# Performance work log

Measured on AMD Instinct MI355X. Metric: run time of the kernel, lower is better.

## Reference

```python
import jax, jax.numpy as jnp
import numpy as np
import math

D_MODEL = 512
N_HEADS = 8
FACTOR = 5
B, L_Q, L_K = 8, 4096, 4096


def setup_inputs() -> dict:
    key = jax.random.key(0)
    ks = jax.random.split(key, 9)
    s = 0.02
    sample_k = max(1, int(FACTOR * math.log(L_K + 1)))  # 41
    return {
        "query": jax.random.normal(ks[0], (B, L_Q, D_MODEL), jnp.float32),
        "key_in": jax.random.normal(ks[1], (B, L_K, D_MODEL), jnp.float32),
        "value": jax.random.normal(ks[2], (B, L_K, D_MODEL), jnp.float32),
        "W_Q": jax.random.normal(ks[3], (D_MODEL, D_MODEL), jnp.float32) * s,
        "W_K": jax.random.normal(ks[4], (D_MODEL, D_MODEL), jnp.float32) * s,
        "W_V": jax.random.normal(ks[5], (D_MODEL, D_MODEL), jnp.float32) * s,
        "W_out": jax.random.normal(ks[6], (D_MODEL, D_MODEL), jnp.float32) * s,
        "b_out": jnp.zeros((D_MODEL,), jnp.float32),
        "sample_idx": jax.random.randint(ks[8], (L_Q, sample_k), 0, L_K),
    }


def reference(query, key_in, value, W_Q, W_K, W_V, W_out, b_out, sample_idx):
    b, lq, _ = query.shape
    lk = key_in.shape[1]
    H = N_HEADS
    E = D_MODEL // H
    # projections -> [B, H, L, E]
    Q = (query @ W_Q).reshape(b, lq, H, E).transpose(0, 2, 1, 3)
    K = (key_in @ W_K).reshape(b, lk, H, E).transpose(0, 2, 1, 3)
    V = (value @ W_V).reshape(b, lk, H, E).transpose(0, 2, 1, 3)

    u = max(1, int(FACTOR * math.log(lq + 1)))  # top-u queries (41)

    # sparsity proxy M(q_i, K) on randomly sampled keys
    K_sample = K[:, :, sample_idx, :]                      # [B,H,L_Q,S,E]
    QK_sample = jnp.einsum('bhqe,bhqse->bhqs', Q, K_sample)
    M = QK_sample.max(axis=-1) - QK_sample.mean(axis=-1)   # [B,H,L_Q]
    _, M_top = jax.lax.top_k(M, u)                         # [B,H,u]

    # attention for the top-u queries only
    Q_reduce = jnp.take_along_axis(Q, M_top[..., None], axis=2)  # [B,H,u,E]
    scale = 1.0 / math.sqrt(E)
    scores = jnp.einsum('bhue,bhke->bhuk', Q_reduce, K) * scale
    attn = jax.nn.softmax(scores, axis=-1)  # dropout is identity (eval)
    ctx_top = jnp.einsum('bhuk,bhke->bhue', attn, V)       # [B,H,u,E]

    # mean-value context for the lazy queries, scatter-update the active ones
    ctx = jnp.broadcast_to(V.mean(axis=2, keepdims=True), (b, H, lq, E))
    bi = jnp.arange(b)[:, None, None]
    hi = jnp.arange(H)[None, :, None]
    ctx = ctx.at[bi, hi, M_top].set(ctx_top)

    ctx = ctx.transpose(0, 2, 1, 3).reshape(b, lq, H * E)
    return ctx @ W_out + b_out
```

## Files before the change

### kernel.cpp

```cpp
#include <hip/hip_runtime.h>
#include <cstdint>
#include <cstddef>

#define D_MODEL 512
#define NHEADS  8
#define EDIM    64
#define BATCH   8
#define LSEQ    4096

typedef unsigned short u16;
typedef __attribute__((ext_vector_type(8))) short short8;
typedef __attribute__((ext_vector_type(4))) float f32x4;

__device__ __forceinline__ u16 bf16_rne(float x) {
  unsigned int u = __float_as_uint(x);
  u += 0x7FFFu + ((u >> 16) & 1u);
  return (u16)(u >> 16);
}
__device__ __forceinline__ void split2(float x, u16& h, u16& l) {
  h = bf16_rne(x);
  float hf = __uint_as_float((unsigned int)h << 16);
  l = bf16_rne(x - hf);
}

__global__ __launch_bounds__(256) void cvt_w(
    const float* __restrict__ W0, const float* __restrict__ W1,
    const float* __restrict__ W2, const float* __restrict__ W3,
    u16* __restrict__ out) {
  const float* W = (blockIdx.z == 0) ? W0 : ((blockIdx.z == 1) ? W1 :
                   ((blockIdx.z == 2) ? W2 : W3));
  u16* P = out + (size_t)blockIdx.z * 524288;
  __shared__ float tile[64][65];
  const int k0 = blockIdx.x * 64, n0 = blockIdx.y * 64;
  const int t = threadIdx.x;
  const int tr = t >> 4, tc = (t & 15) * 4;
#pragma unroll
  for (int j = 0; j < 4; ++j) {
    int kr = tr + j * 16;
    float4 v = *(const float4*)(W + (size_t)(k0 + kr) * 512 + n0 + tc);
    tile[kr][tc + 0] = v.x; tile[kr][tc + 1] = v.y;
    tile[kr][tc + 2] = v.z; tile[kr][tc + 3] = v.w;
  }
  __syncthreads();
#pragma unroll
  for (int j = 0; j < 4; ++j) {
    int nr = tr + j * 16;
    ushort4 h, l;
    split2(tile[tc + 0][nr], h.x, l.x);
    split2(tile[tc + 1][nr], h.y, l.y);
    split2(tile[tc + 2][nr], h.z, l.z);
    split2(tile[tc + 3][nr], h.w, l.w);
    size_t off = (size_t)(n0 + nr) * 512 + k0 + tc;
    *(ushort4*)(P + off) = h;
    *(ushort4*)(P + 262144 + off) = l;
  }
}

__device__ __forceinline__ void gld_lds16(const char* g, char* l) {
  __builtin_amdgcn_global_load_lds((const __attribute__((address_space(1))) void*)g,
                                   (__attribute__((address_space(3))) void*)l, 16, 0, 0);
}

__global__ __launch_bounds__(256, 2) void gemm_fused(
    const float* __restrict__ X, const u16* __restrict__ WP,
    float* __restrict__ Y) {
  __shared__ u16 Ah[128 * 40];
  __shared__ u16 Al[128 * 40];
  __shared__ u16 Bh[128 * 32];
  __shared__ u16 Bl[128 * 32];
  const int tid = threadIdx.x;
  const int lane = tid & 63, wv = tid >> 6;
  const int wm = (wv & 1) * 64, wn = (wv >> 1) * 64;
  const int bn = blockIdx.x * 128, bm = blockIdx.y * 128;
  const int fr = lane & 15, quad = lane >> 4;
  const int sRow = tid >> 2, sColB = (tid & 3) * 16;
  const int ar = tid >> 1, ac = (tid & 1) * 16;

  f32x4 acc[16];
#pragma unroll
  for (int i = 0; i < 16; ++i) acc[i] = (f32x4){0.f, 0.f, 0.f, 0.f};

  const u16* Wh = WP;
  const u16* Wl = WP + 262144;
  const float* Arow = X + (size_t)(bm + ar) * 512 + ac;

  union V8 { ushort4 v4[2]; short8 v8; };

  for (int kk = 0; kk < 16; ++kk) {
    float4 x0 = *(const float4*)(Arow + kk * 32);
    float4 x1 = *(const float4*)(Arow + kk * 32 + 4);
    float4 x2 = *(const float4*)(Arow + kk * 32 + 8);
    float4 x3 = *(const float4*)(Arow + kk * 32 + 12);
#pragma unroll
    for (int j = 0; j < 2; ++j) {
      const size_t rB = (size_t)(bn + j * 64 + sRow) * 512 + kk * 32;
      const int lo = (j * 256 + wv * 64) * 16;
      gld_lds16((const char*)(Wh + rB) + sColB, (char*)Bh + lo);
      gld_lds16((const char*)(Wl + rB) + sColB, (char*)Bl + lo);
    }
    V8 h0, l0, h1, l1;
    split2(x0.x, h0.v4[0].x, l0.v4[0].x);
    split2(x0.y, h0.v4[0].y, l0.v4[0].y);
    split2(x0.z, h0.v4[0].z, l0.v4[0].z);
    split2(x0.w, h0.v4[0].w, l0.v4[0].w);
    split2(x1.x, h0.v4[1].x, l0.v4[1].x);
    split2(x1.y, h0.v4[1].y, l0.v4[1].y);
    split2(x1.z, h0.v4[1].z, l0.v4[1].z);
    split2(x1.w, h0.v4[1].w, l0.v4[1].w);
    split2(x2.x, h1.v4[0].x, l1.v4[0].x);
    split2(x2.y, h1.v4[0].y, l1.v4[0].y);
    split2(x2.z, h1.v4[0].z, l1.v4[0].z);
    split2(x2.w, h1.v4[0].w, l1.v4[0].w);
    split2(x3.x, h1.v4[1].x, l1.v4[1].x);
    split2(x3.y, h1.v4[1].y, l1.v4[1].y);
    split2(x3.z, h1.v4[1].z, l1.v4[1].z);
    split2(x3.w, h1.v4[1].w, l1.v4[1].w);
    *(short8*)&Ah[ar * 40 + ac]     = h0.v8;
    *(short8*)&Ah[ar * 40 + ac + 8] = h1.v8;
    *(short8*)&Al[ar * 40 + ac]     = l0.v8;
    *(short8*)&Al[ar * 40 + ac + 8] = l1.v8;
    __syncthreads();
    short8 ah[4], al[4], bh[4], bl[4];
#pragma unroll
    for (int mi = 0; mi < 4; ++mi) {
      ah[mi] = *(const short8*)&Ah[(wm + mi * 16 + fr) * 40 + quad * 8];
      al[mi] = *(const short8*)&Al[(wm + mi * 16 + fr) * 40 + quad * 8];
    }
#pragma unroll
    for (int ni = 0; ni < 4; ++ni) {
      bh[ni] = *(const short8*)&Bh[(wn + ni * 16 + fr) * 32 + quad * 8];
      bl[ni] = *(const short8*)&Bl[(wn + ni * 16 + fr) * 32 + quad * 8];
    }
#pragma unroll
    for (int mi = 0; mi < 4; ++mi)
#pragma unroll
      for (int ni = 0; ni < 4; ++ni)
        acc[mi * 4 + ni] = __builtin_amdgcn_mfma_f32_16x16x32_bf16(
            ah[mi], bh[ni], acc[mi * 4 + ni], 0, 0, 0);
#pragma unroll
    for (int mi = 0; mi < 4; ++mi)
#pragma unroll
      for (int ni = 0; ni < 4; ++ni)
        acc[mi * 4 + ni] = __builtin_amdgcn_mfma_f32_16x16x32_bf16(
            ah[mi], bl[ni], acc[mi * 4 + ni], 0, 0, 0);
#pragma unroll
    for (int mi = 0; mi < 4; ++mi)
#pragma unroll
      for (int ni = 0; ni < 4; ++ni)
        acc[mi * 4 + ni] = __builtin_amdgcn_mfma_f32_16x16x32_bf16(
            al[mi], bh[ni], acc[mi * 4 + ni], 0, 0, 0);
    __syncthreads();
  }
#pragma unroll
  for (int mi = 0; mi < 4; ++mi)
#pragma unroll
    for (int ni = 0; ni < 4; ++ni) {
      const f32x4 a = acc[mi * 4 + ni];
      float* yp = Y + (size_t)(bm + wm + mi * 16 + quad * 4) * 512 + (bn + wn + ni * 16 + fr);
#pragma unroll
      for (int r = 0; r < 4; ++r) yp[(size_t)r * 512] = a[r];
    }
}

__global__ __launch_bounds__(256) void qk_sample_half(
    const float* __restrict__ Q, const float* __restrict__ K,
    const int* __restrict__ sidx, float* __restrict__ M, int S, int hg) {
  const int blk = blockIdx.x;
  const int lane = threadIdx.x & 63;
  const int b = blk & 7;
  const int q = ((blk >> 3) << 2) + (threadIdx.x >> 6);
  const int s = lane >> 5;
  const int hl = (lane >> 3) & 3;
  const int d = lane & 7;
  const int h = hg * 4 + hl;
  const int col = hg * 256 + hl * 64 + d * 8;

  const float* Qp = Q + ((size_t)b * LSEQ + q) * D_MODEL + col;
  const float4 q0 = *(const float4*)Qp;
  const float4 q1 = *(const float4*)(Qp + 4);
  const float* Kb = K + (size_t)b * LSEQ * D_MODEL + col;
  const int* sp = sidx + (size_t)q * S;

  auto spclamp = [&](int j) -> int {
    int jj = j + s;
    return sp[(jj < S) ? jj : (S - 1)];
  };

  int i0 = spclamp(0), i1 = spclamp(2), i2 = spclamp(4), i3 = spclamp(6);
  const float* p0 = Kb + (size_t)i0 * D_MODEL;
  float4 a0 = *(const float4*)p0, b0 = *(const float4*)(p0 + 4);
  const float* p1 = Kb + (size_t)i1 * D_MODEL;
  float4 a1 = *(const float4*)p1, b1 = *(const float4*)(p1 + 4);
  const float* p2 = Kb + (size_t)i2 * D_MODEL;
  float4 a2 = *(const float4*)p2, b2 = *(const float4*)(p2 + 4);

  float mx = -3.4e38f, sum = 0.0f;
  for (int j = 0; j < S; j += 2) {
    const float4 ca = a0, cb = b0;
    a0 = a1; b0 = b1; a1 = a2; b1 = b2;
    const float* pn = Kb + (size_t)i3 * D_MODEL;
    a2 = *(const float4*)pn;
    b2 = *(const float4*)(pn + 4);
    i3 = spclamp(j + 8);
    float p = ca.x * q0.x + ca.y * q0.y + ca.z * q0.z + ca.w * q0.w +
              cb.x * q1.x + cb.y * q1.y + cb.z * q1.z + cb.w * q1.w;
    p += __shfl_xor(p, 1, 64);
    p += __shfl_xor(p, 2, 64);
    p += __shfl_xor(p, 4, 64);
    if (j + s < S) {
      mx = fmaxf(mx, p);
      sum += p;
    }
  }
  mx = fmaxf(mx, __shfl_xor(mx, 32, 64));
  sum += __shfl_xor(sum, 32, 64);
  if (s == 0 && d == 0)
    M[((size_t)(b * NHEADS + h)) * LSEQ + q] = mx - sum / (float)S;
}

__global__ __launch_bounds__(256) void topk_kernel(
    const float* __restrict__ M, int* __restrict__ Mtop, int U) {
  __shared__ float vals[LSEQ];
  __shared__ float rmax[256];
  __shared__ int ridx[256];
  int bh = blockIdx.x;
  int t = threadIdx.x;
  for (int i = t; i < LSEQ; i += 256) vals[i] = M[(size_t)bh * LSEQ + i];
  __syncthreads();
  for (int it = 0; it < U; ++it) {
    float best = -3.4e38f; int bi = -1;
    for (int i = t; i < LSEQ; i += 256) {
      float v = vals[i];
      if (v > best) { best = v; bi = i; }
    }
    rmax[t] = best; ridx[t] = bi;
    __syncthreads();
    for (int s = 128; s > 0; s >>= 1) {
      if (t < s) {
        if (rmax[t + s] > rmax[t]) { rmax[t] = rmax[t + s]; ridx[t] = ridx[t + s]; }
      }
      __syncthreads();
    }
    if (t == 0) {
      Mtop[(size_t)bh * U + it] = ridx[0];
      vals[ridx[0]] = -3.4e38f;
    }
    __syncthreads();
  }
}

__global__ __launch_bounds__(256, 2) void attn_flash(
    const float* __restrict__ Q, const float* __restrict__ K,
    const float* __restrict__ V, const int* __restrict__ Mtop,
    float* __restrict__ part_ctx, float* __restrict__ part_m,
    float* __restrict__ part_l, int U, int nsplit, int chunks_per_block) {
  __shared__ u16 KhS[64 * 72];
  __shared__ u16 KlS[64 * 72];
  __shared__ float VsS[64 * 68];
  const int bh = blockIdx.y, split = blockIdx.x;
  const int h = bh & (NHEADS - 1), b = bh >> 3;
  const int t = threadIdx.x, w = t >> 6, lane = t & 63;
  const int fr = lane & 15, quad = lane >> 4;

  const int qi = w * 16 + fr;
  const int qrow = (qi < U) ? Mtop[(size_t)bh * U + qi] : Mtop[(size_t)bh * U];
  const float4* Qr = (const float4*)(Q + ((size_t)(b * LSEQ) + qrow) * D_MODEL + h * EDIM);
  float4 qa = Qr[quad * 2], qb = Qr[quad * 2 + 1];
  float4 qc = Qr[quad * 2 + 8], qd = Qr[quad * 2 + 9];
  short8 qh0, ql0, qh1, ql1;
  {
    u16 hh, ll;
    split2(qa.x, hh, ll); qh0[0] = (short)hh; ql0[0] = (short)ll;
    split2(qa.y, hh, ll); qh0[1] = (short)hh; ql0[1] = (short)ll;
    split2(qa.z, hh, ll); qh0[2] = (short)hh; ql0[2] = (short)ll;
    split2(qa.w, hh, ll); qh0[3] = (short)hh; ql0[3] = (short)ll;
    split2(qb.x, hh, ll); qh0[4] = (short)hh; ql0[4] = (short)ll;
    split2(qb.y, hh, ll); qh0[5] = (short)hh; ql0[5] = (short)ll;
    split2(qb.z, hh, ll); qh0[6] = (short)hh; ql0[6] = (short)ll;
    split2(qb.w, hh, ll); qh0[7] = (short)hh; ql0[7] = (short)ll;
    split2(qc.x, hh, ll); qh1[0] = (short)hh; ql1[0] = (short)ll;
    split2(qc.y, hh, ll); qh1[1] = (short)hh; ql1[1] = (short)ll;
    split2(qc.z, hh, ll); qh1[2] = (short)hh; ql1[2] = (short)ll;
    split2(qc.w, hh, ll); qh1[3] = (short)hh; ql1[3] = (short)ll;
    split2(qd.x, hh, ll); qh1[4] = (short)hh; ql1[4] = (short)ll;
    split2(qd.y, hh, ll); qh1[5] = (short)hh; ql1[5] = (short)ll;
    split2(qd.z, hh, ll); qh1[6] = (short)hh; ql1[6] = (short)ll;
    split2(qd.w, hh, ll); qh1[7] = (short)hh; ql1[7] = (short)ll;
  }

  float4 c4[16];
#pragma unroll
  for (int i = 0; i < 16; ++i) c4[i] = make_float4(0.f, 0.f, 0.f, 0.f);
  float m = -1e30f, l = 0.0f;

  const int r = t >> 2, cg = t & 3;

  const int k_base = split * (chunks_per_block * 64);
  for (int c = 0; c < chunks_per_block; ++c) {
    const int k0 = k_base + c * 64;
    const float4* Kg4 = (const float4*)(K + ((size_t)(b * LSEQ) + k0 + r) * D_MODEL + h * EDIM);
    const float4* Vg4 = (const float4*)(V + ((size_t)(b * LSEQ) + k0 + r) * D_MODEL + h * EDIM);
#pragma unroll
    for (int i = 0; i < 4; ++i) {
      const int f4 = cg + 4 * i;
      float4 kv = Kg4[f4];
      float4 vv = Vg4[f4];
      ushort4 hh, ll;
      split2(kv.x, hh.x, ll.x);
      split2(kv.y, hh.y, ll.y);
      split2(kv.z, hh.z, ll.z);
      split2(kv.w, hh.w, ll.w);
      *(ushort4*)&KhS[r * 72 + f4 * 4] = hh;
      *(ushort4*)&KlS[r * 72 + f4 * 4] = ll;
      *(float4*)&VsS[r * 68 + f4 * 4] = vv;
    }
    __syncthreads();

    f32x4 acc[4];
#pragma unroll
    for (int mt = 0; mt < 4; ++mt) acc[mt] = (f32x4){0.f, 0.f, 0.f, 0.f};
#pragma unroll
    for (int mt = 0; mt < 4; ++mt) {
      short8 kh = *(const short8*)&KhS[(mt * 16 + fr) * 72 + quad * 8];
      short8 kl = *(const short8*)&KlS[(mt * 16 + fr) * 72 + quad * 8];
      acc[mt] = __builtin_amdgcn_mfma_f32_16x16x32_bf16(kh, qh0, acc[mt], 0, 0, 0);
      acc[mt] = __builtin_amdgcn_mfma_f32_16x16x32_bf16(kh, ql0, acc[mt], 0, 0, 0);
      acc[mt] = __builtin_amdgcn_mfma_f32_16x16x32_bf16(kl, qh0, acc[mt], 0, 0, 0);
    }
#pragma unroll
    for (int mt = 0; mt < 4; ++mt) {
      short8 kh = *(const short8*)&KhS[(mt * 16 + fr) * 72 + 32 + quad * 8];
      short8 kl = *(const short8*)&KlS[(mt * 16 + fr) * 72 + 32 + quad * 8];
      acc[mt] = __builtin_amdgcn_mfma_f32_16x16x32_bf16(kh, qh1, acc[mt], 0, 0, 0);
      acc[mt] = __builtin_amdgcn_mfma_f32_16x16x32_bf16(kh, ql1, acc[mt], 0, 0, 0);
      acc[mt] = __builtin_amdgcn_mfma_f32_16x16x32_bf16(kl, qh1, acc[mt], 0, 0, 0);
    }

    float cm = -3.4e38f;
#pragma unroll
    for (int mt = 0; mt < 4; ++mt) {
#pragma unroll
      for (int rr = 0; rr < 4; ++rr) {
        float s = acc[mt][rr] * 0.125f;
        acc[mt][rr] = s;
        cm = fmaxf(cm, s);
      }
    }
    cm = fmaxf(cm, __shfl_xor(cm, 16, 64));
    cm = fmaxf(cm, __shfl_xor(cm, 32, 64));
    float mn = fmaxf(m, cm);
    if (mn > m) {
      float f = __expf(m - mn);
      l *= f;
#pragma unroll
      for (int i = 0; i < 16; ++i) {
        c4[i].x *= f; c4[i].y *= f; c4[i].z *= f; c4[i].w *= f;
      }
      m = mn;
    }
    float psum = 0.0f;
#pragma unroll
    for (int mt = 0; mt < 4; ++mt) {
#pragma unroll
      for (int rr = 0; rr < 4; ++rr) {
        float p = __expf(acc[mt][rr] - m);
        acc[mt][rr] = p;
        psum += p;
      }
    }
    l += psum;

#pragma unroll
    for (int mt = 0; mt < 4; ++mt) {
#pragma unroll
      for (int rr = 0; rr < 4; ++rr) {
        const int krow = mt * 16 + quad * 4 + rr;
        const float4* vr = (const float4*)&VsS[krow * 68];
        const float p = acc[mt][rr];
#pragma unroll
        for (int i = 0; i < 16; ++i) {
          float4 vv = vr[i];
          c4[i].x += p * vv.x; c4[i].y += p * vv.y;
          c4[i].z += p * vv.z; c4[i].w += p * vv.w;
        }
      }
    }
    __syncthreads();
  }

#pragma unroll
  for (int i = 0; i < 16; ++i) {
    c4[i].x += __shfl_xor(c4[i].x, 16, 64);
    c4[i].y += __shfl_xor(c4[i].y, 16, 64);
    c4[i].z += __shfl_xor(c4[i].z, 16, 64);
    c4[i].w += __shfl_xor(c4[i].w, 16, 64);
    c4[i].x += __shfl_xor(c4[i].x, 32, 64);
    c4[i].y += __shfl_xor(c4[i].y, 32, 64);
    c4[i].z += __shfl_xor(c4[i].z, 32, 64);
    c4[i].w += __shfl_xor(c4[i].w, 32, 64);
  }
  l += __shfl_xor(l, 16, 64);
  l += __shfl_xor(l, 32, 64);

  if (quad == 0 && qi < U) {
    part_m[(size_t)(bh * nsplit + split) * 64 + qi] = m;
    part_l[(size_t)(bh * nsplit + split) * 64 + qi] = l;
  }
  float* pc = part_ctx + (size_t)(bh * nsplit + split) * 4096;
  if (quad == 0) {
#pragma unroll
    for (int ii = 0; ii < 16; ++ii) pc[ii * 64 + qi] = (&c4[ii >> 2].x)[ii & 3];
  } else if (quad == 1) {
#pragma unroll
    for (int ii = 0; ii < 16; ++ii) pc[(16 + ii) * 64 + qi] = (&c4[4 + (ii >> 2)].x)[ii & 3];
  } else if (quad == 2) {
#pragma unroll
    for (int ii = 0; ii < 16; ++ii) pc[(32 + ii) * 64 + qi] = (&c4[8 + (ii >> 2)].x)[ii & 3];
  } else {
#pragma unroll
    for (int ii = 0; ii < 16; ++ii) pc[(48 + ii) * 64 + qi] = (&c4[12 + (ii >> 2)].x)[ii & 3];
  }
}

__global__ __launch_bounds__(256) void attn_combine(
    const float* __restrict__ part_ctx, const float* __restrict__ part_m,
    const float* __restrict__ part_l, float* __restrict__ ctxTop,
    int U, int nsplit) {
  __shared__ float F[16][64];
  const int bh = blockIdx.x;
  const int t = threadIdx.x, lane = t & 63, grp = t >> 6;
  if (grp == 0) {
    float M = -3.4e38f;
    for (int s = 0; s < nsplit; ++s)
      M = fmaxf(M, part_m[(size_t)(bh * nsplit + s) * 64 + lane]);
    float L = 0.0f;
    for (int s = 0; s < nsplit; ++s)
      L += part_l[(size_t)(bh * nsplit + s) * 64 + lane] *
           __expf(part_m[(size_t)(bh * nsplit + s) * 64 + lane] - M);
    float invL = 1.0f / L;
    for (int s = 0; s < nsplit; ++s)
      F[s][lane] = __expf(part_m[(size_t)(bh * nsplit + s) * 64 + lane] - M) * invL;
  }
  __syncthreads();
  for (int ei = 0; ei < 16; ++ei) {
    int e = grp * 16 + ei;
    float acc = 0.0f;
    for (int s = 0; s < nsplit; ++s)
      acc += F[s][lane] * part_ctx[(size_t)(bh * nsplit + s) * 4096 + e * 64 + lane];
    if (lane < U) ctxTop[((size_t)bh * U + lane) * 64 + e] = acc;
  }
}

__global__ __launch_bounds__(256) void vmean_kernel(
    const float* __restrict__ V, float* __restrict__ Vm) {
  __shared__ float part[4][EDIM];
  int bh = blockIdx.x;
  int h = bh & (NHEADS - 1), b = bh >> 3;
  int t = threadIdx.x;
  int e = t & 63, c = t >> 6;
  float s = 0.0f;
  for (int k = c * (LSEQ / 4); k < (c + 1) * (LSEQ / 4); ++k)
    s += V[((size_t)b * LSEQ + k) * D_MODEL + h * EDIM + e];
  part[c][e] = s;
  __syncthreads();
  if (c == 0)
    Vm[(size_t)bh * EDIM + e] =
        (part[0][e] + part[1][e] + part[2][e] + part[3][e]) * (1.0f / (float)LSEQ);
}

__global__ __launch_bounds__(256) void base_out_kernel(
    const float* __restrict__ Vm, const float* __restrict__ Wout,
    const float* __restrict__ bout, float* __restrict__ base) {
  __shared__ float cb[D_MODEL];
  int b = blockIdx.x;
  int t = threadIdx.x;
  for (int d = t; d < D_MODEL; d += 256) cb[d] = Vm[(size_t)b * D_MODEL + d];
  __syncthreads();
  for (int n = t; n < D_MODEL; n += 256) {
    float s = bout[n];
    for (int d = 0; d < D_MODEL; ++d) s += cb[d] * Wout[(size_t)d * D_MODEL + n];
    base[(size_t)b * D_MODEL + n] = s;
  }
}

__global__ __launch_bounds__(256) void fill_out(
    const float* __restrict__ base, float* __restrict__ out) {
  size_t i = (size_t)blockIdx.x * 256 + threadIdx.x;
  int n4 = (int)(i & 127);
  size_t bq = i >> 7;
  int b = (int)(bq >> 12);
  float4 v = ((const float4*)base)[(size_t)b * 128 + n4];
  ((float4*)out)[i] = v;
}

__global__ __launch_bounds__(256, 1) void delta_out_mfma(
    const float* __restrict__ ctxTop, const float* __restrict__ Vm,
    const int* __restrict__ Mtop, const u16* __restrict__ WoutTP,
    float* __restrict__ out, int U) {
  __shared__ u16 Dh[64 * 72];
  __shared__ u16 Dl[64 * 72];
  __shared__ int qr[64];
  const int bh = blockIdx.x;
  const int h = bh & (NHEADS - 1), b = bh >> 3;
  const int t = threadIdx.x, lane = t & 63, wv = t >> 6;
  const int fr = lane & 15, quad = lane >> 4;

  {
    const int r = t >> 2, c0 = (t & 3) * 16;
#pragma unroll
    for (int j = 0; j < 4; ++j) {
      float4 v = make_float4(0.f, 0.f, 0.f, 0.f);
      if (r < U) {
        float4 cv = *(const float4*)(ctxTop + ((size_t)bh * U + r) * EDIM + c0 + j * 4);
        float4 mv = *(const float4*)(Vm + (size_t)bh * EDIM + c0 + j * 4);
        v = make_float4(cv.x - mv.x, cv.y - mv.y, cv.z - mv.z, cv.w - mv.w);
      }
      ushort4 hh, ll;
      split2(v.x, hh.x, ll.x);
      split2(v.y, hh.y, ll.y);
      split2(v.z, hh.z, ll.z);
      split2(v.w, hh.w, ll.w);
      *(ushort4*)&Dh[r * 72 + c0 + j * 4] = hh;
      *(ushort4*)&Dl[r * 72 + c0 + j * 4] = ll;
    }
  }
  if (t < 64) qr[t] = (t < U) ? Mtop[(size_t)bh * U + t] : -1;
  __syncthreads();

  f32x4 acc[32];
#pragma unroll
  for (int i = 0; i < 32; ++i) acc[i] = (f32x4){0.f, 0.f, 0.f, 0.f};

  const u16* Wh = WoutTP;
  const u16* Wl = WoutTP + 262144;

#pragma unroll
  for (int ks = 0; ks < 2; ++ks) {
    short8 a_h[4], a_l[4];
#pragma unroll
    for (int mt = 0; mt < 4; ++mt) {
      a_h[mt] = *(const short8*)&Dh[(mt * 16 + fr) * 72 + ks * 32 + quad * 8];
      a_l[mt] = *(const short8*)&Dl[(mt * 16 + fr) * 72 + ks * 32 + quad * 8];
    }
#pragma unroll
    for (int nt = 0; nt < 8; ++nt) {
      const int n = wv * 128 + nt * 16 + fr;
      const size_t off = (size_t)n * 512 + h * EDIM + ks * 32 + quad * 8;
      short8 b_h = *(const short8*)&Wh[off];
      short8 b_l = *(const short8*)&Wl[off];
#pragma unroll
      for (int mt = 0; mt < 4; ++mt) {
        acc[mt * 8 + nt] = __builtin_amdgcn_mfma_f32_16x16x32_bf16(
            a_h[mt], b_h, acc[mt * 8 + nt], 0, 0, 0);
        acc[mt * 8 + nt] = __builtin_amdgcn_mfma_f32_16x16x32_bf16(
            a_h[mt], b_l, acc[mt * 8 + nt], 0, 0, 0);
        acc[mt * 8 + nt] = __builtin_amdgcn_mfma_f32_16x16x32_bf16(
            a_l[mt], b_h, acc[mt * 8 + nt], 0, 0, 0);
      }
    }
  }

  int qreg[16];
#pragma unroll
  for (int mt = 0; mt < 4; ++mt)
#pragma unroll
    for (int r4 = 0; r4 < 4; ++r4) qreg[mt * 4 + r4] = qr[mt * 16 + quad * 4 + r4];
#pragma unroll
  for (int mt = 0; mt < 4; ++mt)
#pragma unroll
    for (int nt = 0; nt < 8; ++nt) {
      const f32x4 a = acc[mt * 8 + nt];
      const int n = wv * 128 + nt * 16 + fr;
#pragma unroll
      for (int r4 = 0; r4 < 4; ++r4) {
        const int q = qreg[mt * 4 + r4];
        if (q >= 0)
          atomicAdd(out + ((size_t)b * LSEQ + q) * D_MODEL + n, a[r4]);
      }
    }
}

extern "C" void kernel_launch(void* const* d_in, const int* in_sizes, int n_in,
                              void* d_out, int out_size, void* d_ws, size_t ws_size,
                              hipStream_t stream) {
  const float* query  = (const float*)d_in[0];
  const float* key_in = (const float*)d_in[1];
  const float* value  = (const float*)d_in[2];
  const float* W_Q    = (const float*)d_in[3];
  const float* W_K    = (const float*)d_in[4];
  const float* W_V    = (const float*)d_in[5];
  const float* W_out  = (const float*)d_in[6];
  const float* b_out  = (const float*)d_in[7];
  const int*   sidx   = (const int*)d_in[8];
  float* out = (float*)d_out;

  const int S = in_sizes[8] / LSEQ;
  const int U = S;

  char* ws = (char*)d_ws;
  size_t o = 0;
  float* Qf     = (float*)(ws + o); o += (size_t)BATCH * LSEQ * D_MODEL * 4;
  float* Kf     = (float*)(ws + o); o += (size_t)BATCH * LSEQ * D_MODEL * 4;
  float* Vf     = (float*)(ws + o); o += (size_t)BATCH * LSEQ * D_MODEL * 4;
  int*   Mtop   = (int*)  (ws + o); o += ((size_t)64 * U * 4 + 255) & ~255ULL;
  float* ctxTop = (float*)(ws + o); o += ((size_t)64 * U * EDIM * 4 + 255) & ~255ULL;
  float* Vm     = (float*)(ws + o); o += 16384;
  float* baseO  = (float*)(ws + o); o += 16384;
  u16*   Wpl    = (u16*)  (ws + o); o += (size_t)4 * 524288 * 2;
  size_t unionOff = o;

  float* M = (float*)(ws + unionOff);
  int nsplit = 16;
  for (;;) {
    size_t need = unionOff + 2 * ((size_t)64 * nsplit * 64 * 4)
                  + (size_t)64 * nsplit * 4096 * 4;
    if (need <= ws_size || nsplit == 1) break;
    nsplit >>= 1;
  }
  float* part_m   = (float*)(ws + unionOff);
  float* part_l   = part_m + (size_t)64 * nsplit * 64;
  float* part_ctx = part_l + (size_t)64 * nsplit * 64;
  const int chunks_per_block = 64 / nsplit;

  cvt_w<<<dim3(8, 8, 4), 256, 0, stream>>>(W_Q, W_K, W_V, W_out, Wpl);
  gemm_fused<<<dim3(4, 256), 256, 0, stream>>>(query,  Wpl,                       Qf);
  gemm_fused<<<dim3(4, 256), 256, 0, stream>>>(key_in, Wpl + (size_t)1 * 524288,  Kf);
  gemm_fused<<<dim3(4, 256), 256, 0, stream>>>(value,  Wpl + (size_t)2 * 524288,  Vf);

  qk_sample_half<<<(BATCH * LSEQ) / 4, 256, 0, stream>>>(Qf, Kf, sidx, M, S, 0);
  qk_sample_half<<<(BATCH * LSEQ) / 4, 256, 0, stream>>>(Qf, Kf, sidx, M, S, 1);
  topk_kernel<<<BATCH * NHEADS, 256, 0, stream>>>(M, Mtop, U);
  attn_flash<<<dim3(nsplit, BATCH * NHEADS), 256, 0, stream>>>(
      Qf, Kf, Vf, Mtop, part_ctx, part_m, part_l, U, nsplit, chunks_per_block);
  attn_combine<<<BATCH * NHEADS, 256, 0, stream>>>(
      part_ctx, part_m, part_l, ctxTop, U, nsplit);
  vmean_kernel<<<BATCH * NHEADS, 256, 0, stream>>>(Vf, Vm);
  base_out_kernel<<<BATCH, 256, 0, stream>>>(Vm, W_out, b_out, baseO);
  fill_out<<<(BATCH * LSEQ * (D_MODEL / 4)) / 256, 256, 0, stream>>>(baseO, out);
  delta_out_mfma<<<BATCH * NHEADS, 256, 0, stream>>>(
      ctxTop, Vm, Mtop, Wpl + (size_t)3 * 524288, out, U);
}
```

Before: 779.2 us.

## Double-buffer projection GEMM, merge QKV launches, speed up topk and vmean

The projection GEMM now double-buffers its LDS tiles so the next K-slice's global loads and bf16 split run alongside the MFMAs of the current slice. The three Q/K/V GEMMs are merged into one launch through blockIdx.z. The top-k selection replaces its shared-memory tree reduction with wave shuffles and explicit tie-breaking. The V-mean kernel is split over 8 chunks per head with atomicAdd into a zero-filled buffer, and the qk_sample prefetch depth is cut from 3 rows to 2. Double buffering doubles LDS use and may hurt occupancy at 2 blocks per CU, and the float atomics make the V-mean summation order nondeterministic.

```diff
diff --git a/kernel.cpp b/kernel.cpp
--- a/kernel.cpp
+++ b/kernel.cpp
@@ -62,12 +62,18 @@
 }
 
 __global__ __launch_bounds__(256, 2) void gemm_fused(
-    const float* __restrict__ X, const u16* __restrict__ WP,
-    float* __restrict__ Y) {
-  __shared__ u16 Ah[128 * 40];
-  __shared__ u16 Al[128 * 40];
-  __shared__ u16 Bh[128 * 32];
-  __shared__ u16 Bl[128 * 32];
+    const float* __restrict__ X0, const float* __restrict__ X1,
+    const float* __restrict__ X2, const u16* __restrict__ WPbase,
+    float* __restrict__ Y0, float* __restrict__ Y1, float* __restrict__ Y2) {
+  __shared__ u16 Ah[2][128 * 40];
+  __shared__ u16 Al[2][128 * 40];
+  __shared__ u16 Bh[2][128 * 32];
+  __shared__ u16 Bl[2][128 * 32];
+  const int z = blockIdx.z;
+  const float* X = (z == 0) ? X0 : ((z == 1) ? X1 : X2);
+  float* Y = (z == 0) ? Y0 : ((z == 1) ? Y1 : Y2);
+  const u16* WP = WPbase + (size_t)z * 524288;
+
   const int tid = threadIdx.x;
   const int lane = tid & 63, wv = tid >> 6;
   const int wm = (wv & 1) * 64, wn = (wv >> 1) * 64;
@@ -86,17 +92,17 @@
 
   union V8 { ushort4 v4[2]; short8 v8; };
 
-  for (int kk = 0; kk < 16; ++kk) {
-    float4 x0 = *(const float4*)(Arow + kk * 32);
-    float4 x1 = *(const float4*)(Arow + kk * 32 + 4);
-    float4 x2 = *(const float4*)(Arow + kk * 32 + 8);
-    float4 x3 = *(const float4*)(Arow + kk * 32 + 12);
+  {
+    float4 x0 = *(const float4*)(Arow);
+    float4 x1 = *(const float4*)(Arow + 4);
+    float4 x2 = *(const float4*)(Arow + 8);
+    float4 x3 = *(const float4*)(Arow + 12);
 #pragma unroll
     for (int j = 0; j < 2; ++j) {
-      const size_t rB = (size_t)(bn + j * 64 + sRow) * 512 + kk * 32;
+      const size_t rB = (size_t)(bn + j * 64 + sRow) * 512;
       const int lo = (j * 256 + wv * 64) * 16;
-      gld_lds16((const char*)(Wh + rB) + sColB, (char*)Bh + lo);
-      gld_lds16((const char*)(Wl + rB) + sColB, (char*)Bl + lo);
+      gld_lds16((const char*)(Wh + rB) + sColB, (char*)Bh[0] + lo);
+      gld_lds16((const char*)(Wl + rB) + sColB, (char*)Bl[0] + lo);
     }
     V8 h0, l0, h1, l1;
     split2(x0.x, h0.v4[0].x, l0.v4[0].x);
@@ -115,40 +121,81 @@
     split2(x3.y, h1.v4[1].y, l1.v4[1].y);
     split2(x3.z, h1.v4[1].z, l1.v4[1].z);
     split2(x3.w, h1.v4[1].w, l1.v4[1].w);
-    *(short8*)&Ah[ar * 40 + ac]     = h0.v8;
-    *(short8*)&Ah[ar * 40 + ac + 8] = h1.v8;
-    *(short8*)&Al[ar * 40 + ac]     = l0.v8;
-    *(short8*)&Al[ar * 40 + ac + 8] = l1.v8;
-    __syncthreads();
-    short8 ah[4], al[4], bh[4], bl[4];
+    *(short8*)&Ah[0][ar * 40 + ac]     = h0.v8;
+    *(short8*)&Ah[0][ar * 40 + ac + 8] = h1.v8;
+    *(short8*)&Al[0][ar * 40 + ac]     = l0.v8;
+    *(short8*)&Al[0][ar * 40 + ac + 8] = l1.v8;
+  }
+  __syncthreads();
+
+  for (int kk = 0; kk < 16; ++kk) {
+    const int cur = kk & 1, nxt = cur ^ 1;
+    float4 x0, x1, x2, x3;
+    if (kk < 15) {
+      x0 = *(const float4*)(Arow + (kk + 1) * 32);
+      x1 = *(const float4*)(Arow + (kk + 1) * 32 + 4);
+      x2 = *(const float4*)(Arow + (kk + 1) * 32 + 8);
+      x3 = *(const float4*)(Arow + (kk + 1) * 32 + 12);
+#pragma unroll
+      for (int j = 0; j < 2; ++j) {
+        const size_t rB = (size_t)(bn + j * 64 + sRow) * 512 + (kk + 1) * 32;
+        const int lo = (j * 256 + wv * 64) * 16;
+        gld_lds16((const char*)(Wh + rB) + sColB, (char*)Bh[nxt] + lo);
+        gld_lds16((const char*)(Wl + rB) + sColB, (char*)Bl[nxt] + lo);
+      }
+    }
+    short8 ah[4], al[4], bh4[4], bl4[4];
 #pragma unroll
     for (int mi = 0; mi < 4; ++mi) {
-      ah[mi] = *(const short8*)&Ah[(wm + mi * 16 + fr) * 40 + quad * 8];
-      al[mi] = *(const short8*)&Al[(wm + mi * 16 + fr) * 40 + quad * 8];
+      ah[mi] = *(const short8*)&Ah[cur][(wm + mi * 16 + fr) * 40 + quad * 8];
+      al[mi] = *(const short8*)&Al[cur][(wm + mi * 16 + fr) * 40 + quad * 8];
     }
 #pragma unroll
     for (int ni = 0; ni < 4; ++ni) {
-      bh[ni] = *(const short8*)&Bh[(wn + ni * 16 + fr) * 32 + quad * 8];
-      bl[ni] = *(const short8*)&Bl[(wn + ni * 16 + fr) * 32 + quad * 8];
+      bh4[ni] = *(const short8*)&Bh[cur][(wn + ni * 16 + fr) * 32 + quad * 8];
+      bl4[ni] = *(const short8*)&Bl[cur][(wn + ni * 16 + fr) * 32 + quad * 8];
     }
 #pragma unroll
     for (int mi = 0; mi < 4; ++mi)
 #pragma unroll
       for (int ni = 0; ni < 4; ++ni)
         acc[mi * 4 + ni] = __builtin_amdgcn_mfma_f32_16x16x32_bf16(
-            ah[mi], bh[ni], acc[mi * 4 + ni], 0, 0, 0);
+            ah[mi], bh4[ni], acc[mi * 4 + ni], 0, 0, 0);
 #pragma unroll
     for (int mi = 0; mi < 4; ++mi)
 #pragma unroll
       for (int ni = 0; ni < 4; ++ni)
         acc[mi * 4 + ni] = __builtin_amdgcn_mfma_f32_16x16x32_bf16(
-            ah[mi], bl[ni], acc[mi * 4 + ni], 0, 0, 0);
+            ah[mi], bl4[ni], acc[mi * 4 + ni], 0, 0, 0);
 #pragma unroll
     for (int mi = 0; mi < 4; ++mi)
 #pragma unroll
       for (int ni = 0; ni < 4; ++ni)
         acc[mi * 4 + ni] = __builtin_amdgcn_mfma_f32_16x16x32_bf16(
-            al[mi], bh[ni], acc[mi * 4 + ni], 0, 0, 0);
+            al[mi], bh4[ni], acc[mi * 4 + ni], 0, 0, 0);
+    if (kk < 15) {
+      V8 h0, l0, h1, l1;
+      split2(x0.x, h0.v4[0].x, l0.v4[0].x);
+      split2(x0.y, h0.v4[0].y, l0.v4[0].y);
+      split2(x0.z, h0.v4[0].z, l0.v4[0].z);
+      split2(x0.w, h0.v4[0].w, l0.v4[0].w);
+      split2(x1.x, h0.v4[1].x, l0.v4[1].x);
+      split2(x1.y, h0.v4[1].y, l0.v4[1].y);
+      split2(x1.z, h0.v4[1].z, l0.v4[1].z);
+      split2(x1.w, h0.v4[1].w, l0.v4[1].w);
+      split2(x2.x, h1.v4[0].x, l1.v4[0].x);
+      split2(x2.y, h1.v4[0].y, l1.v4[0].y);
+      split2(x2.z, h1.v4[0].z, l1.v4[0].z);
+      split2(x2.w, h1.v4[0].w, l1.v4[0].w);
+      split2(x3.x, h1.v4[1].x, l1.v4[1].x);
+      split2(x3.y, h1.v4[1].y, l1.v4[1].y);
+      split2(x3.z, h1.v4[1].z, l1.v4[1].z);
+      split2(x3.w, h1.v4[1].w, l1.v4[1].w);
+      *(short8*)&Ah[nxt][ar * 40 + ac]     = h0.v8;
+      *(short8*)&Ah[nxt][ar * 40 + ac + 8] = h1.v8;
+      *(short8*)&Al[nxt][ar * 40 + ac]     = l0.v8;
+      *(short8*)&Al[nxt][ar * 40 + ac + 8] = l1.v8;
+    }
     __syncthreads();
   }
 #pragma unroll
@@ -181,27 +228,24 @@
   const float* Kb = K + (size_t)b * LSEQ * D_MODEL + col;
   const int* sp = sidx + (size_t)q * S;
 
-  auto spclamp = [&](int j) -> int {
+  auto rowp = [&](int j) -> const float* {
     int jj = j + s;
-    return sp[(jj < S) ? jj : (S - 1)];
+    int row = sp[(jj < S) ? jj : (S - 1)];
+    return Kb + (size_t)row * D_MODEL;
   };
 
-  int i0 = spclamp(0), i1 = spclamp(2), i2 = spclamp(4), i3 = spclamp(6);
-  const float* p0 = Kb + (size_t)i0 * D_MODEL;
-  float4 a0 = *(const float4*)p0, b0 = *(const float4*)(p0 + 4);
-  const float* p1 = Kb + (size_t)i1 * D_MODEL;
-  float4 a1 = *(const float4*)p1, b1 = *(const float4*)(p1 + 4);
-  const float* p2 = Kb + (size_t)i2 * D_MODEL;
-  float4 a2 = *(const float4*)p2, b2 = *(const float4*)(p2 + 4);
+  const float* pr0 = rowp(0);
+  float4 a0 = *(const float4*)pr0, b0 = *(const float4*)(pr0 + 4);
+  const float* pr1 = rowp(2);
+  float4 a1 = *(const float4*)pr1, b1 = *(const float4*)(pr1 + 4);
 
   float mx = -3.4e38f, sum = 0.0f;
   for (int j = 0; j < S; j += 2) {
     const float4 ca = a0, cb = b0;
-    a0 = a1; b0 = b1; a1 = a2; b1 = b2;
-    const float* pn = Kb + (size_t)i3 * D_MODEL;
-    a2 = *(const float4*)pn;
-    b2 = *(const float4*)(pn + 4);
-    i3 = spclamp(j + 8);
+    a0 = a1; b0 = b1;
+    const float* pn = rowp(j + 4);
+    a1 = *(const float4*)pn;
+    b1 = *(const float4*)(pn + 4);
     float p = ca.x * q0.x + ca.y * q0.y + ca.z * q0.z + ca.w * q0.w +
               cb.x * q1.x + cb.y * q1.y + cb.z * q1.z + cb.w * q1.w;
     p += __shfl_xor(p, 1, 64);
@@ -221,29 +265,36 @@
 __global__ __launch_bounds__(256) void topk_kernel(
     const float* __restrict__ M, int* __restrict__ Mtop, int U) {
   __shared__ float vals[LSEQ];
-  __shared__ float rmax[256];
-  __shared__ int ridx[256];
+  __shared__ float wbest[4];
+  __shared__ int widx[4];
   int bh = blockIdx.x;
   int t = threadIdx.x;
+  const int w = t >> 6, lane = t & 63;
   for (int i = t; i < LSEQ; i += 256) vals[i] = M[(size_t)bh * LSEQ + i];
   __syncthreads();
   for (int it = 0; it < U; ++it) {
-    float best = -3.4e38f; int bi = -1;
+    float best = -3.4e38f; int bi = 0x7fffffff;
     for (int i = t; i < LSEQ; i += 256) {
       float v = vals[i];
       if (v > best) { best = v; bi = i; }
     }
-    rmax[t] = best; ridx[t] = bi;
+#pragma unroll
+    for (int o = 1; o < 64; o <<= 1) {
+      float ov = __shfl_xor(best, o, 64);
+      int oi = __shfl_xor(bi, o, 64);
+      if (ov > best || (ov == best && oi < bi)) { best = ov; bi = oi; }
+    }
+    if (lane == 0) { wbest[w] = best; widx[w] = bi; }
     __syncthreads();
-    for (int s = 128; s > 0; s >>= 1) {
-      if (t < s) {
-        if (rmax[t + s] > rmax[t]) { rmax[t] = rmax[t + s]; ridx[t] = ridx[t + s]; }
-      }
-      __syncthreads();
-    }
     if (t == 0) {
-      Mtop[(size_t)bh * U + it] = ridx[0];
-      vals[ridx[0]] = -3.4e38f;
+      float B = wbest[0]; int I = widx[0];
+#pragma unroll
+      for (int w2 = 1; w2 < 4; ++w2)
+        if (wbest[w2] > B || (wbest[w2] == B && widx[w2] < I)) {
+          B = wbest[w2]; I = widx[w2];
+        }
+      Mtop[(size_t)bh * U + it] = I;
+      vals[I] = -3.4e38f;
     }
     __syncthreads();
   }
@@ -451,21 +502,23 @@
   }
 }
 
-__global__ __launch_bounds__(256) void vmean_kernel(
+__global__ __launch_bounds__(256) void vmean_part(
     const float* __restrict__ V, float* __restrict__ Vm) {
   __shared__ float part[4][EDIM];
-  int bh = blockIdx.x;
-  int h = bh & (NHEADS - 1), b = bh >> 3;
-  int t = threadIdx.x;
-  int e = t & 63, c = t >> 6;
+  const int bh = blockIdx.x, chunk = blockIdx.y;
+  const int h = bh & (NHEADS - 1), b = bh >> 3;
+  const int t = threadIdx.x;
+  const int e = t & 63, c = t >> 6;
   float s = 0.0f;
-  for (int k = c * (LSEQ / 4); k < (c + 1) * (LSEQ / 4); ++k)
+  const int k0 = chunk * 512 + c * 128;
+  for (int k = k0; k < k0 + 128; ++k)
     s += V[((size_t)b * LSEQ + k) * D_MODEL + h * EDIM + e];
   part[c][e] = s;
   __syncthreads();
   if (c == 0)
-    Vm[(size_t)bh * EDIM + e] =
-        (part[0][e] + part[1][e] + part[2][e] + part[3][e]) * (1.0f / (float)LSEQ);
+    atomicAdd(&Vm[(size_t)bh * EDIM + e],
+              (part[0][e] + part[1][e] + part[2][e] + part[3][e]) *
+                  (1.0f / (float)LSEQ));
 }
 
 __global__ __launch_bounds__(256) void base_out_kernel(
@@ -623,9 +676,8 @@
   const int chunks_per_block = 64 / nsplit;
 
   cvt_w<<<dim3(8, 8, 4), 256, 0, stream>>>(W_Q, W_K, W_V, W_out, Wpl);
-  gemm_fused<<<dim3(4, 256), 256, 0, stream>>>(query,  Wpl,                       Qf);
-  gemm_fused<<<dim3(4, 256), 256, 0, stream>>>(key_in, Wpl + (size_t)1 * 524288,  Kf);
-  gemm_fused<<<dim3(4, 256), 256, 0, stream>>>(value,  Wpl + (size_t)2 * 524288,  Vf);
+  gemm_fused<<<dim3(4, 256, 3), 256, 0, stream>>>(
+      query, key_in, value, Wpl, Qf, Kf, Vf);
 
   qk_sample_half<<<(BATCH * LSEQ) / 4, 256, 0, stream>>>(Qf, Kf, sidx, M, S, 0);
   qk_sample_half<<<(BATCH * LSEQ) / 4, 256, 0, stream>>>(Qf, Kf, sidx, M, S, 1);
@@ -634,7 +686,8 @@
       Qf, Kf, Vf, Mtop, part_ctx, part_m, part_l, U, nsplit, chunks_per_block);
   attn_combine<<<BATCH * NHEADS, 256, 0, stream>>>(
       part_ctx, part_m, part_l, ctxTop, U, nsplit);
-  vmean_kernel<<<BATCH * NHEADS, 256, 0, stream>>>(Vf, Vm);
+  hipMemsetAsync(Vm, 0, (size_t)BATCH * NHEADS * EDIM * 4, stream);
+  vmean_part<<<dim3(BATCH * NHEADS, 8), 256, 0, stream>>>(Vf, Vm);
   base_out_kernel<<<BATCH, 256, 0, stream>>>(Vm, W_out, b_out, baseO);
   fill_out<<<(BATCH * LSEQ * (D_MODEL / 4)) / 256, 256, 0, stream>>>(baseO, out);
   delta_out_mfma<<<BATCH * NHEADS, 256, 0, stream>>>(
```

After: 827.9 us. 1.06x slower.
